# Performance work log

Hardware: AMD Instinct MI355X
Metric: run time of the kernel (lower is better)

Reference implementation:

```python
import jax, jax.numpy as jnp
import numpy as np

N = 50000
E = 800000
IN_C = 128
HID_C = 128
OUT_C = 128
N_CLS = 40


def setup_inputs() -> dict:
    key = jax.random.key(0)
    ks = jax.random.split(key, 12)
    x = jax.random.normal(ks[0], (N, IN_C), dtype=jnp.float32)
    edge_index = jax.random.randint(ks[1], (2, E), 0, N, dtype=jnp.int64)
    s = 1.0 / np.sqrt(IN_C)
    W_l1 = jax.random.uniform(ks[2], (IN_C, HID_C), jnp.float32, -s, s)
    W_r1 = jax.random.uniform(ks[3], (IN_C, HID_C), jnp.float32, -s, s)
    b1 = jax.random.uniform(ks[4], (HID_C,), jnp.float32, -s, s)
    s2 = 1.0 / np.sqrt(HID_C)
    W_l2 = jax.random.uniform(ks[5], (HID_C, OUT_C), jnp.float32, -s2, s2)
    W_r2 = jax.random.uniform(ks[6], (HID_C, OUT_C), jnp.float32, -s2, s2)
    b2 = jax.random.uniform(ks[7], (OUT_C,), jnp.float32, -s2, s2)
    s3 = 1.0 / np.sqrt(OUT_C)
    W_c = jax.random.uniform(ks[8], (OUT_C, N_CLS), jnp.float32, -s3, s3)
    b_c = jax.random.uniform(ks[9], (N_CLS,), jnp.float32, -s3, s3)
    return {"x": x, "edge_index": edge_index, "W_l1": W_l1, "W_r1": W_r1,
            "b1": b1, "W_l2": W_l2, "W_r2": W_r2, "b2": b2,
            "W_c": W_c, "b_c": b_c}


def _mean_aggregate(x, src, dst, deg_inv):
    # gather source node features over edges, scatter-mean to dst nodes
    msg = x[src]  # [E, C]
    agg = jax.ops.segment_sum(msg, dst, num_segments=N)  # [N, C]
    return agg * deg_inv[:, None]


def _sage_conv(x, src, dst, deg_inv, W_l, W_r, b):
    # PyG SAGEConv (mean aggr): out = agg @ W_l + x @ W_r + b
    agg = _mean_aggregate(x, src, dst, deg_inv)
    return agg @ W_l + x @ W_r + b


def reference(x, edge_index, W_l1, W_r1, b1, W_l2, W_r2, b2, W_c, b_c):
    src, dst = edge_index[0], edge_index[1]
    deg = jax.ops.segment_sum(jnp.ones((E,), jnp.float32), dst, num_segments=N)
    deg_inv = jnp.where(deg > 0, 1.0 / jnp.maximum(deg, 1.0), 0.0)
    h = jax.nn.relu(_sage_conv(x, src, dst, deg_inv, W_l1, W_r1, b1))
    h = jax.nn.relu(_sage_conv(h, src, dst, deg_inv, W_l2, W_r2, b2))
    return h @ W_c + b_c
```

## Files before the change

kernel.cpp:

```cpp
#include <hip/hip_runtime.h>

#define N_NODES 50000
#define N_EDGES 800000
#define C 128
#define NCLS 40
#define KB 98
#define BCAP 9216
#define WLD 264

typedef short bf16x8 __attribute__((ext_vector_type(8)));
typedef float f32x4 __attribute__((ext_vector_type(4)));
typedef unsigned short ushort_t;

__device__ __forceinline__ unsigned short f32_to_bf16(float f) {
    union { float f; unsigned u; } c; c.f = f;
    unsigned r = (c.u + 0x7FFFu + ((c.u >> 16) & 1u)) >> 16;
    return (unsigned short)r;
}
__device__ __forceinline__ float bf_lo(unsigned u) {
    union { unsigned u; float f; } c; c.u = u << 16; return c.f;
}
__device__ __forceinline__ float bf_hi(unsigned u) {
    union { unsigned u; float f; } c; c.u = u & 0xffff0000u; return c.f;
}
__device__ __forceinline__ unsigned pack_bf16(float lo, float hi) {
    return (unsigned)f32_to_bf16(lo) | ((unsigned)f32_to_bf16(hi) << 16);
}
__device__ __forceinline__ bf16x8 as_bf(uint4 u) {
    union { uint4 u; bf16x8 b; } c; c.u = u; return c.b;
}
__device__ __forceinline__ void acc8(float* a, uint4 v) {
    a[0] += bf_lo(v.x); a[1] += bf_hi(v.x); a[2] += bf_lo(v.y); a[3] += bf_hi(v.y);
    a[4] += bf_lo(v.z); a[5] += bf_hi(v.z); a[6] += bf_lo(v.w); a[7] += bf_hi(v.w);
}
__device__ __forceinline__ void acc8m(float* a, uint4 v, float mk) {
    a[0] += mk * bf_lo(v.x); a[1] += mk * bf_hi(v.x); a[2] += mk * bf_lo(v.y); a[3] += mk * bf_hi(v.y);
    a[4] += mk * bf_lo(v.z); a[5] += mk * bf_hi(v.z); a[6] += mk * bf_lo(v.w); a[7] += mk * bf_hi(v.w);
}

__global__ __launch_bounds__(256)
void convert_all(const float* __restrict__ Wl1, const float* __restrict__ Wr1,
                 const float* __restrict__ Wl2, const float* __restrict__ Wr2,
                 const float* __restrict__ Wc,  const float* __restrict__ x,
                 ushort_t* __restrict__ Wbf1, ushort_t* __restrict__ Wbf2,
                 ushort_t* __restrict__ Wcb,  ushort_t* __restrict__ xb) {
    int b = blockIdx.x;
    int tid = threadIdx.x;
    if (b < 256) {
        const float* Wl = (b < 128) ? Wl1 : Wl2;
        const float* Wr = (b < 128) ? Wr1 : Wr2;
        ushort_t* Bpre  = (b < 128) ? Wbf1 : Wbf2;
        int idx = (b & 127) * 256 + tid;
        int n = idx >> 8;
        int k = idx & 255;
        float v = (k < 128) ? Wl[k * 128 + n] : Wr[(k - 128) * 128 + n];
        Bpre[n * 256 + k] = f32_to_bf16(v);
    } else if (b < 280) {
        int idx = (b - 256) * 256 + tid;
        if (idx < 48 * 128) {
            int n = idx >> 7;
            int k = idx & 127;
            float v = (n < NCLS) ? Wc[k * NCLS + n] : 0.f;
            Wcb[idx] = f32_to_bf16(v);
        }
    } else {
        int idx = (b - 280) * 256 + tid;
        const float4 v0 = *(const float4*)&x[idx * 8];
        const float4 v1 = *(const float4*)&x[idx * 8 + 4];
        uint4 o;
        o.x = pack_bf16(v0.x, v0.y);
        o.y = pack_bf16(v0.z, v0.w);
        o.z = pack_bf16(v1.x, v1.y);
        o.w = pack_bf16(v1.z, v1.w);
        ((uint4*)xb)[idx] = o;
    }
}

__global__ __launch_bounds__(256)
void bin_kernel(const int* __restrict__ src, const int* __restrict__ dst,
                int* __restrict__ bucket_cnt, unsigned* __restrict__ bucket_data) {
    __shared__ int lh[KB];
    int tid = threadIdx.x;
    int e0 = blockIdx.x * 4096;
    if (tid < KB) lh[tid] = 0;
    __syncthreads();
#pragma unroll
    for (int j = 0; j < 16; ++j) {
        int e = e0 + j * 256 + tid;
        if (e < N_EDGES) atomicAdd(&lh[dst[e] >> 9], 1);
    }
    __syncthreads();
    if (tid < KB) lh[tid] = atomicAdd(&bucket_cnt[tid], lh[tid]);
    __syncthreads();
#pragma unroll
    for (int j = 0; j < 16; ++j) {
        int e = e0 + j * 256 + tid;
        if (e < N_EDGES) {
            int d = dst[e];
            int b = d >> 9;
            int pos = atomicAdd(&lh[b], 1);
            if (pos < BCAP)
                bucket_data[b * BCAP + pos] = (unsigned)src[e] | ((unsigned)(d & 511) << 16);
        }
    }
}

__global__ __launch_bounds__(256)
void build_kernel(const int* __restrict__ bucket_cnt, const unsigned* __restrict__ bucket_data,
                  int* __restrict__ row_ptr, ushort_t* __restrict__ csr16,
                  int* __restrict__ perm) {
    __shared__ int wt[4];
    __shared__ int wt2[4];
    __shared__ int sbases[128];
    __shared__ int hist[512];
    __shared__ int loff[512];
    __shared__ int dhist[64];
    __shared__ ushort_t lcsr[BCAP];
    int tid = threadIdx.x;
    int b = blockIdx.x;
    int n0 = b << 9;
    int nb = min(512, N_NODES - n0);

    int v = 0, x = 0;
    if (tid < 128) {
        v = (tid < KB) ? bucket_cnt[tid] : 0;
        x = v;
#pragma unroll
        for (int off = 1; off < 64; off <<= 1) {
            int t = __shfl_up(x, off, 64);
            if ((tid & 63) >= off) x += t;
        }
        if ((tid & 63) == 63) wt[tid >> 6] = x;
    }
    hist[tid] = 0; hist[tid + 256] = 0;
    __syncthreads();
    if (tid < 128) sbases[tid] = x - v + ((tid >= 64) ? wt[0] : 0);
    __syncthreads();
    int base = sbases[b];
    int ecnt = min(bucket_cnt[b], BCAP);

    for (int i = tid; i < ecnt; i += 256)
        atomicAdd(&hist[bucket_data[b * BCAP + i] >> 16], 1);
    __syncthreads();

    int h0 = hist[2 * tid], h1 = hist[2 * tid + 1];
    int s = h0 + h1;
    int y = s;
#pragma unroll
    for (int off = 1; off < 64; off <<= 1) {
        int t = __shfl_up(y, off, 64);
        if ((tid & 63) >= off) y += t;
    }
    if ((tid & 63) == 63) wt2[tid >> 6] = y;
    __syncthreads();
    int add = 0;
    for (int j = 0; j < (tid >> 6); ++j) add += wt2[j];
    int ex = y + add - s;
    loff[2 * tid] = ex;
    loff[2 * tid + 1] = ex + h0;
    __syncthreads();

    for (int n = tid; n < nb; n += 256) row_ptr[n0 + n] = base + loff[n];
    if (b == KB - 1 && tid == 0) row_ptr[N_NODES] = N_EDGES;
    __syncthreads();

    for (int i = tid; i < ecnt; i += 256) {
        unsigned e = bucket_data[b * BCAP + i];
        int pos = atomicAdd(&loff[e >> 16], 1);
        lcsr[pos] = (ushort_t)(e & 0xFFFFu);
    }
    __syncthreads();
    for (int i = tid; i < ecnt; i += 256) csr16[base + i] = lcsr[i];

    if (tid < 64) dhist[tid] = 0;
    for (int p = tid; p < 512; p += 256) perm[(b << 9) + p] = -1;
    __syncthreads();
    int na = 2 * tid, nbb = 2 * tid + 1;
    int c0 = min(h0, 63), c1 = min(h1, 63);
    if (na < nb)  atomicAdd(&dhist[c0], 1);
    if (nbb < nb) atomicAdd(&dhist[c1], 1);
    __syncthreads();
    if (tid < 64) {
        int v2 = dhist[tid];
        int xs = v2;
#pragma unroll
        for (int off = 1; off < 64; off <<= 1) {
            int t = __shfl_up(xs, off, 64);
            if (tid >= off) xs += t;
        }
        dhist[tid] = xs - v2;
    }
    __syncthreads();
    if (na < nb)  { int pos = atomicAdd(&dhist[c0], 1); perm[(b << 9) + pos] = n0 + na; }
    if (nbb < nb) { int pos = atomicAdd(&dhist[c1], 1); perm[(b << 9) + pos] = n0 + nbb; }
}

__global__ __launch_bounds__(256)
void gather_kernel(const ushort_t* __restrict__ feat,
                   const int* __restrict__ row_ptr,
                   const ushort_t* __restrict__ csr16,
                   const int* __restrict__ perm,
                   ushort_t* __restrict__ agg) {
    const int tid = threadIdx.x;
    const int q = tid & 15;
    const int g = tid >> 4;
    int slot = blockIdx.x * 16 + g;
    int node = perm[slot];
    if (node < 0) return;
    int beg = row_ptr[node], end = row_ptr[node + 1];
    int deg = end - beg;
    const uint4* fb = (const uint4*)feat;

    float a0[8], a1[8], a2[8], a3[8];
#pragma unroll
    for (int j = 0; j < 8; ++j) { a0[j] = 0.f; a1[j] = 0.f; a2[j] = 0.f; a3[j] = 0.f; }

    int n8 = deg >> 3;
    int s0 = 0, s1 = 0, s2 = 0, s3 = 0, s4 = 0, s5 = 0, s6 = 0, s7 = 0;
    if (n8 > 0) {
        s0 = csr16[beg];     s1 = csr16[beg + 1]; s2 = csr16[beg + 2]; s3 = csr16[beg + 3];
        s4 = csr16[beg + 4]; s5 = csr16[beg + 5]; s6 = csr16[beg + 6]; s7 = csr16[beg + 7];
    }
    for (int it = 0; it < n8; ++it) {
        uint4 v0 = fb[s0 * 16 + q];
        uint4 v1 = fb[s1 * 16 + q];
        uint4 v2 = fb[s2 * 16 + q];
        uint4 v3 = fb[s3 * 16 + q];
        uint4 v4 = fb[s4 * 16 + q];
        uint4 v5 = fb[s5 * 16 + q];
        uint4 v6 = fb[s6 * 16 + q];
        uint4 v7 = fb[s7 * 16 + q];
        if (it + 1 < n8) {
            int bs = beg + (it + 1) * 8;
            s0 = csr16[bs];     s1 = csr16[bs + 1]; s2 = csr16[bs + 2]; s3 = csr16[bs + 3];
            s4 = csr16[bs + 4]; s5 = csr16[bs + 5]; s6 = csr16[bs + 6]; s7 = csr16[bs + 7];
        }
        acc8(a0, v0); acc8(a1, v1); acc8(a2, v2); acc8(a3, v3);
        acc8(a0, v4); acc8(a1, v5); acc8(a2, v6); acc8(a3, v7);
    }
    int i = beg + n8 * 8;
    if (i + 4 <= end) {
        int t0 = csr16[i], t1 = csr16[i + 1], t2 = csr16[i + 2], t3 = csr16[i + 3];
        uint4 v0 = fb[t0 * 16 + q];
        uint4 v1 = fb[t1 * 16 + q];
        uint4 v2 = fb[t2 * 16 + q];
        uint4 v3 = fb[t3 * 16 + q];
        acc8(a0, v0); acc8(a1, v1); acc8(a2, v2); acc8(a3, v3);
        i += 4;
    }
    int rem = end - i;
    if (rem > 0) {
        int t0 = csr16[i];
        int t1 = csr16[i + (rem > 1 ? 1 : 0)];
        int t2 = csr16[i + (rem > 2 ? 2 : 0)];
        uint4 v0 = fb[t0 * 16 + q];
        uint4 v1 = fb[t1 * 16 + q];
        uint4 v2 = fb[t2 * 16 + q];
        acc8(a0, v0);
        acc8m(a1, v1, rem > 1 ? 1.f : 0.f);
        acc8m(a2, v2, rem > 2 ? 1.f : 0.f);
    }
    float di = deg > 0 ? 1.f / (float)deg : 0.f;
    float r[8];
#pragma unroll
    for (int j = 0; j < 8; ++j) r[j] = (a0[j] + a1[j] + a2[j] + a3[j]) * di;
    uint4 o;
    o.x = pack_bf16(r[0], r[1]);
    o.y = pack_bf16(r[2], r[3]);
    o.z = pack_bf16(r[4], r[5]);
    o.w = pack_bf16(r[6], r[7]);
    *(uint4*)&agg[node * C + q * 8] = o;
}

#define HLD 136
template<int CLS>
__global__ __launch_bounds__(256)
void gemm_layer(const ushort_t* __restrict__ agg,
                const ushort_t* __restrict__ feat,
                const ushort_t* __restrict__ Bpre,
                const float* __restrict__ bias,
                ushort_t* __restrict__ hout,
                const ushort_t* __restrict__ Wcb,
                const float* __restrict__ bc,
                float* __restrict__ out) {
    __shared__ ushort_t Wlds[128 * WLD];
    const int tid = threadIdx.x;
    const int r0 = blockIdx.x * 64;
    const int w = tid >> 6, lane = tid & 63, m = lane & 15, quad = lane >> 4;

#pragma unroll
    for (int i = 0; i < 16; ++i) {
        int idx = i * 256 + tid;
        int row = idx >> 5, c32 = idx & 31;
        *(uint4*)&Wlds[row * WLD + c32 * 8] = *(const uint4*)&Bpre[row * 256 + c32 * 8];
    }

    int rg = r0 + w * 16 + m; if (rg >= N_NODES) rg = N_NODES - 1;
    uint4 afa[4], aff[4];
#pragma unroll
    for (int kc = 0; kc < 4; ++kc) afa[kc] = *(const uint4*)&agg[rg * C + kc * 32 + quad * 8];
#pragma unroll
    for (int kc = 0; kc < 4; ++kc) aff[kc] = *(const uint4*)&feat[rg * C + kc * 32 + quad * 8];

    __syncthreads();

    f32x4 acc[8];
#pragma unroll
    for (int t = 0; t < 8; ++t) acc[t] = (f32x4){0.f, 0.f, 0.f, 0.f};

#pragma unroll
    for (int kc = 0; kc < 8; ++kc) {
        bf16x8 af = (kc < 4) ? as_bf(afa[kc]) : as_bf(aff[kc - 4]);
#pragma unroll
        for (int t = 0; t < 8; ++t) {
            bf16x8 bf = *(const bf16x8*)&Wlds[(t * 16 + m) * WLD + kc * 32 + quad * 8];
            acc[t] = __builtin_amdgcn_mfma_f32_16x16x32_bf16(af, bf, acc[t], 0, 0, 0);
        }
    }

    if (CLS == 0) {
#pragma unroll
        for (int t = 0; t < 8; ++t) {
            int colv = t * 16 + m;
            float bv = bias[colv];
#pragma unroll
            for (int reg = 0; reg < 4; ++reg) {
                int rs = r0 + w * 16 + quad * 4 + reg;
                if (rs < N_NODES) {
                    float vv = fmaxf(acc[t][reg] + bv, 0.f);
                    hout[rs * C + colv] = f32_to_bf16(vv);
                }
            }
        }
    } else {
        ushort_t* h2L = Wlds;
        ushort_t* WcL = Wlds + 64 * HLD;
        __syncthreads();
#pragma unroll
        for (int t = 0; t < 8; ++t) {
            int colv = t * 16 + m;
            float bv = bias[colv];
#pragma unroll
            for (int reg = 0; reg < 4; ++reg) {
                int rl = w * 16 + quad * 4 + reg;
                float vv = fmaxf(acc[t][reg] + bv, 0.f);
                h2L[rl * HLD + colv] = f32_to_bf16(vv);
            }
        }
#pragma unroll
        for (int i = 0; i < 3; ++i) {
            int slot = tid + i * 256;
            int n = slot >> 4, c16 = slot & 15;
            *(uint4*)&WcL[n * HLD + c16 * 8] = *(const uint4*)&Wcb[n * C + c16 * 8];
        }
        __syncthreads();
        f32x4 acc2[3];
#pragma unroll
        for (int t = 0; t < 3; ++t) acc2[t] = (f32x4){0.f, 0.f, 0.f, 0.f};
#pragma unroll
        for (int kc = 0; kc < 4; ++kc) {
            bf16x8 af = *(const bf16x8*)&h2L[(w * 16 + m) * HLD + kc * 32 + quad * 8];
#pragma unroll
            for (int t = 0; t < 3; ++t) {
                bf16x8 bf = *(const bf16x8*)&WcL[(t * 16 + m) * HLD + kc * 32 + quad * 8];
                acc2[t] = __builtin_amdgcn_mfma_f32_16x16x32_bf16(af, bf, acc2[t], 0, 0, 0);
            }
        }
#pragma unroll
        for (int t = 0; t < 3; ++t) {
            int col = t * 16 + m;
            if (col < NCLS) {
                float bvv = bc[col];
#pragma unroll
                for (int reg = 0; reg < 4; ++reg) {
                    int rs = r0 + w * 16 + quad * 4 + reg;
                    if (rs < N_NODES) out[rs * NCLS + col] = acc2[t][reg] + bvv;
                }
            }
        }
    }
}

extern "C" void kernel_launch(void* const* d_in, const int* in_sizes, int n_in,
                              void* d_out, int out_size, void* d_ws, size_t ws_size,
                              hipStream_t stream) {
    const float* x   = (const float*)d_in[0];
    const int*   ei  = (const int*)d_in[1];
    const float* Wl1 = (const float*)d_in[2];
    const float* Wr1 = (const float*)d_in[3];
    const float* b1  = (const float*)d_in[4];
    const float* Wl2 = (const float*)d_in[5];
    const float* Wr2 = (const float*)d_in[6];
    const float* b2  = (const float*)d_in[7];
    const float* Wc  = (const float*)d_in[8];
    const float* bc  = (const float*)d_in[9];
    const int* srcI = ei;
    const int* dstI = ei + N_EDGES;
    float* out = (float*)d_out;

    ushort_t* xb   = (ushort_t*)d_ws;
    ushort_t* h1b  = xb + (size_t)N_NODES * C;
    ushort_t* Wbf1 = h1b + (size_t)N_NODES * C;
    ushort_t* Wbf2 = Wbf1 + 32768;
    ushort_t* Wcb  = Wbf2 + 32768;
    ushort_t* csr16 = Wcb + 6144;
    int* bucket_cnt = (int*)(csr16 + N_EDGES);
    int* row_ptr    = bucket_cnt + 128;
    unsigned* bucket_data = (unsigned*)(row_ptr + N_NODES + 1);
    int* perm = (int*)(bucket_data + (size_t)KB * BCAP);
    ushort_t* aggb = (ushort_t*)(perm + KB * 512);

    convert_all<<<280 + (N_NODES * C / 8 + 255) / 256, 256, 0, stream>>>(
        Wl1, Wr1, Wl2, Wr2, Wc, x, Wbf1, Wbf2, Wcb, xb);

    hipMemsetAsync(bucket_cnt, 0, 128 * sizeof(int), stream);
    bin_kernel<<<(N_EDGES + 4095) / 4096, 256, 0, stream>>>(srcI, dstI, bucket_cnt, bucket_data);
    build_kernel<<<KB, 256, 0, stream>>>(bucket_cnt, bucket_data, row_ptr, csr16, perm);

    gather_kernel<<<KB * 512 / 16, 256, 0, stream>>>(xb, row_ptr, csr16, perm, aggb);
    gemm_layer<0><<<(N_NODES + 63) / 64, 256, 0, stream>>>(
        aggb, xb, Wbf1, b1, h1b, nullptr, nullptr, nullptr);

    gather_kernel<<<KB * 512 / 16, 256, 0, stream>>>(h1b, row_ptr, csr16, perm, aggb);
    gemm_layer<1><<<(N_NODES + 63) / 64, 256, 0, stream>>>(
        aggb, h1b, Wbf2, b2, nullptr, Wcb, bc, out);
}
```

Before: 222.1 us.

## Globally degree-sort nodes, source-sort CSR rows, and persist gather blocks over interleaved tiles

Node ordering for the gather now comes from a global degree histogram. A scan kernel and an atomic perm kernel replace the per-bucket degree sort, so nodes of similar degree are grouped across the whole graph. The build kernel also counting-sorts each bucket's edges by the high byte of the source id before placing them into CSR, so neighbor reads within a row touch nearby feature rows. The gather kernel now runs 784 blocks, each handling four 16-node groups taken from interleaved tiles, with launch bounds set for occupancy. This adds two small launches, a perm memset and extra shared memory in build in exchange for better load balance and locality.

```diff
diff --git a/kernel.cpp b/kernel.cpp
--- a/kernel.cpp
+++ b/kernel.cpp
@@ -7,6 +7,7 @@
 #define KB 98
 #define BCAP 9216
 #define WLD 264
+#define NPERM 50176
 
 typedef short bf16x8 __attribute__((ext_vector_type(8)));
 typedef float f32x4 __attribute__((ext_vector_type(4)));
@@ -108,13 +109,15 @@
 __global__ __launch_bounds__(256)
 void build_kernel(const int* __restrict__ bucket_cnt, const unsigned* __restrict__ bucket_data,
                   int* __restrict__ row_ptr, ushort_t* __restrict__ csr16,
-                  int* __restrict__ perm) {
+                  int* __restrict__ ghist) {
     __shared__ int wt[4];
     __shared__ int wt2[4];
     __shared__ int sbases[128];
     __shared__ int hist[512];
     __shared__ int loff[512];
-    __shared__ int dhist[64];
+    __shared__ int shist[256];
+    __shared__ int scur[256];
+    __shared__ unsigned sorted[BCAP];
     __shared__ ushort_t lcsr[BCAP];
     int tid = threadIdx.x;
     int b = blockIdx.x;
@@ -132,15 +135,41 @@
         }
         if ((tid & 63) == 63) wt[tid >> 6] = x;
     }
-    hist[tid] = 0; hist[tid + 256] = 0;
+    hist[tid] = 0; hist[tid + 256] = 0; shist[tid] = 0;
     __syncthreads();
     if (tid < 128) sbases[tid] = x - v + ((tid >= 64) ? wt[0] : 0);
     __syncthreads();
     int base = sbases[b];
     int ecnt = min(bucket_cnt[b], BCAP);
 
-    for (int i = tid; i < ecnt; i += 256)
-        atomicAdd(&hist[bucket_data[b * BCAP + i] >> 16], 1);
+    for (int i = tid; i < ecnt; i += 256) {
+        unsigned rec = bucket_data[b * BCAP + i];
+        atomicAdd(&shist[(rec & 0xFFFFu) >> 8], 1);
+        atomicAdd(&hist[rec >> 16], 1);
+    }
+    __syncthreads();
+
+    {
+        int v2 = shist[tid];
+        int y2 = v2;
+#pragma unroll
+        for (int off = 1; off < 64; off <<= 1) {
+            int t = __shfl_up(y2, off, 64);
+            if ((tid & 63) >= off) y2 += t;
+        }
+        if ((tid & 63) == 63) wt2[tid >> 6] = y2;
+        __syncthreads();
+        int add = 0;
+        for (int j = 0; j < (tid >> 6); ++j) add += wt2[j];
+        scur[tid] = y2 + add - v2;
+    }
+    __syncthreads();
+
+    for (int i = tid; i < ecnt; i += 256) {
+        unsigned rec = bucket_data[b * BCAP + i];
+        int pos = atomicAdd(&scur[(rec & 0xFFFFu) >> 8], 1);
+        sorted[pos] = rec;
+    }
     __syncthreads();
 
     int h0 = hist[2 * tid], h1 = hist[2 * tid + 1];
@@ -165,37 +194,41 @@
     __syncthreads();
 
     for (int i = tid; i < ecnt; i += 256) {
-        unsigned e = bucket_data[b * BCAP + i];
-        int pos = atomicAdd(&loff[e >> 16], 1);
-        lcsr[pos] = (ushort_t)(e & 0xFFFFu);
+        unsigned rec = sorted[i];
+        int pos = atomicAdd(&loff[rec >> 16], 1);
+        lcsr[pos] = (ushort_t)(rec & 0xFFFFu);
     }
     __syncthreads();
     for (int i = tid; i < ecnt; i += 256) csr16[base + i] = lcsr[i];
 
-    if (tid < 64) dhist[tid] = 0;
-    for (int p = tid; p < 512; p += 256) perm[(b << 9) + p] = -1;
-    __syncthreads();
-    int na = 2 * tid, nbb = 2 * tid + 1;
-    int c0 = min(h0, 63), c1 = min(h1, 63);
-    if (na < nb)  atomicAdd(&dhist[c0], 1);
-    if (nbb < nb) atomicAdd(&dhist[c1], 1);
-    __syncthreads();
-    if (tid < 64) {
-        int v2 = dhist[tid];
-        int xs = v2;
-#pragma unroll
-        for (int off = 1; off < 64; off <<= 1) {
-            int t = __shfl_up(xs, off, 64);
-            if (tid >= off) xs += t;
-        }
-        dhist[tid] = xs - v2;
-    }
-    __syncthreads();
-    if (na < nb)  { int pos = atomicAdd(&dhist[c0], 1); perm[(b << 9) + pos] = n0 + na; }
-    if (nbb < nb) { int pos = atomicAdd(&dhist[c1], 1); perm[(b << 9) + pos] = n0 + nbb; }
+    if (2 * tid < nb)     atomicAdd(&ghist[min(h0, 63)], 1);
+    if (2 * tid + 1 < nb) atomicAdd(&ghist[min(h1, 63)], 1);
+}
+
+__global__ void scan_kernel(const int* __restrict__ ghist, int* __restrict__ gcur) {
+    int t = threadIdx.x;
+    int v = ghist[t];
+    int x = v;
+#pragma unroll
+    for (int off = 1; off < 64; off <<= 1) {
+        int u = __shfl_up(x, off, 64);
+        if (t >= off) x += u;
+    }
+    gcur[t] = x - v;
 }
 
 __global__ __launch_bounds__(256)
+void perm_kernel(const int* __restrict__ row_ptr, int* __restrict__ gcur,
+                 int* __restrict__ perm) {
+    int n = blockIdx.x * 256 + threadIdx.x;
+    if (n < N_NODES) {
+        int deg = row_ptr[n + 1] - row_ptr[n];
+        int pos = atomicAdd(&gcur[min(deg, 63)], 1);
+        perm[pos] = n;
+    }
+}
+
+__global__ __launch_bounds__(256, 4)
 void gather_kernel(const ushort_t* __restrict__ feat,
                    const int* __restrict__ row_ptr,
                    const ushort_t* __restrict__ csr16,
@@ -204,72 +237,77 @@
     const int tid = threadIdx.x;
     const int q = tid & 15;
     const int g = tid >> 4;
-    int slot = blockIdx.x * 16 + g;
-    int node = perm[slot];
-    if (node < 0) return;
-    int beg = row_ptr[node], end = row_ptr[node + 1];
-    int deg = end - beg;
+    int bid = blockIdx.x;
+    int r0 = ((bid & 7) * 98 + (bid >> 3)) * 64;
     const uint4* fb = (const uint4*)feat;
 
-    float a0[8], a1[8], a2[8], a3[8];
-#pragma unroll
-    for (int j = 0; j < 8; ++j) { a0[j] = 0.f; a1[j] = 0.f; a2[j] = 0.f; a3[j] = 0.f; }
-
-    int n8 = deg >> 3;
-    int s0 = 0, s1 = 0, s2 = 0, s3 = 0, s4 = 0, s5 = 0, s6 = 0, s7 = 0;
-    if (n8 > 0) {
-        s0 = csr16[beg];     s1 = csr16[beg + 1]; s2 = csr16[beg + 2]; s3 = csr16[beg + 3];
-        s4 = csr16[beg + 4]; s5 = csr16[beg + 5]; s6 = csr16[beg + 6]; s7 = csr16[beg + 7];
-    }
-    for (int it = 0; it < n8; ++it) {
-        uint4 v0 = fb[s0 * 16 + q];
-        uint4 v1 = fb[s1 * 16 + q];
-        uint4 v2 = fb[s2 * 16 + q];
-        uint4 v3 = fb[s3 * 16 + q];
-        uint4 v4 = fb[s4 * 16 + q];
-        uint4 v5 = fb[s5 * 16 + q];
-        uint4 v6 = fb[s6 * 16 + q];
-        uint4 v7 = fb[s7 * 16 + q];
-        if (it + 1 < n8) {
-            int bs = beg + (it + 1) * 8;
-            s0 = csr16[bs];     s1 = csr16[bs + 1]; s2 = csr16[bs + 2]; s3 = csr16[bs + 3];
-            s4 = csr16[bs + 4]; s5 = csr16[bs + 5]; s6 = csr16[bs + 6]; s7 = csr16[bs + 7];
-        }
-        acc8(a0, v0); acc8(a1, v1); acc8(a2, v2); acc8(a3, v3);
-        acc8(a0, v4); acc8(a1, v5); acc8(a2, v6); acc8(a3, v7);
-    }
-    int i = beg + n8 * 8;
-    if (i + 4 <= end) {
-        int t0 = csr16[i], t1 = csr16[i + 1], t2 = csr16[i + 2], t3 = csr16[i + 3];
-        uint4 v0 = fb[t0 * 16 + q];
-        uint4 v1 = fb[t1 * 16 + q];
-        uint4 v2 = fb[t2 * 16 + q];
-        uint4 v3 = fb[t3 * 16 + q];
-        acc8(a0, v0); acc8(a1, v1); acc8(a2, v2); acc8(a3, v3);
-        i += 4;
-    }
-    int rem = end - i;
-    if (rem > 0) {
-        int t0 = csr16[i];
-        int t1 = csr16[i + (rem > 1 ? 1 : 0)];
-        int t2 = csr16[i + (rem > 2 ? 2 : 0)];
-        uint4 v0 = fb[t0 * 16 + q];
-        uint4 v1 = fb[t1 * 16 + q];
-        uint4 v2 = fb[t2 * 16 + q];
-        acc8(a0, v0);
-        acc8m(a1, v1, rem > 1 ? 1.f : 0.f);
-        acc8m(a2, v2, rem > 2 ? 1.f : 0.f);
-    }
-    float di = deg > 0 ? 1.f / (float)deg : 0.f;
-    float r[8];
-#pragma unroll
-    for (int j = 0; j < 8; ++j) r[j] = (a0[j] + a1[j] + a2[j] + a3[j]) * di;
-    uint4 o;
-    o.x = pack_bf16(r[0], r[1]);
-    o.y = pack_bf16(r[2], r[3]);
-    o.z = pack_bf16(r[4], r[5]);
-    o.w = pack_bf16(r[6], r[7]);
-    *(uint4*)&agg[node * C + q * 8] = o;
+    for (int p = 0; p < 4; ++p) {
+        int node = perm[r0 + p * 16 + g];
+        if (node >= 0) {
+            int beg = row_ptr[node], end = row_ptr[node + 1];
+            int deg = end - beg;
+
+            float a0[8], a1[8], a2[8], a3[8];
+#pragma unroll
+            for (int j = 0; j < 8; ++j) { a0[j] = 0.f; a1[j] = 0.f; a2[j] = 0.f; a3[j] = 0.f; }
+
+            int n8 = deg >> 3;
+            int s0 = 0, s1 = 0, s2 = 0, s3 = 0, s4 = 0, s5 = 0, s6 = 0, s7 = 0;
+            if (n8 > 0) {
+                s0 = csr16[beg];     s1 = csr16[beg + 1]; s2 = csr16[beg + 2]; s3 = csr16[beg + 3];
+                s4 = csr16[beg + 4]; s5 = csr16[beg + 5]; s6 = csr16[beg + 6]; s7 = csr16[beg + 7];
+            }
+            for (int it = 0; it < n8; ++it) {
+                uint4 v0 = fb[s0 * 16 + q];
+                uint4 v1 = fb[s1 * 16 + q];
+                uint4 v2 = fb[s2 * 16 + q];
+                uint4 v3 = fb[s3 * 16 + q];
+                uint4 v4 = fb[s4 * 16 + q];
+                uint4 v5 = fb[s5 * 16 + q];
+                uint4 v6 = fb[s6 * 16 + q];
+                uint4 v7 = fb[s7 * 16 + q];
+                if (it + 1 < n8) {
+                    int bs = beg + (it + 1) * 8;
+                    s0 = csr16[bs];     s1 = csr16[bs + 1]; s2 = csr16[bs + 2]; s3 = csr16[bs + 3];
+                    s4 = csr16[bs + 4]; s5 = csr16[bs + 5]; s6 = csr16[bs + 6]; s7 = csr16[bs + 7];
+                }
+                acc8(a0, v0); acc8(a1, v1); acc8(a2, v2); acc8(a3, v3);
+                acc8(a0, v4); acc8(a1, v5); acc8(a2, v6); acc8(a3, v7);
+            }
+            int i = beg + n8 * 8;
+            if (i + 4 <= end) {
+                int t0 = csr16[i], t1 = csr16[i + 1], t2 = csr16[i + 2], t3 = csr16[i + 3];
+                uint4 v0 = fb[t0 * 16 + q];
+                uint4 v1 = fb[t1 * 16 + q];
+                uint4 v2 = fb[t2 * 16 + q];
+                uint4 v3 = fb[t3 * 16 + q];
+                acc8(a0, v0); acc8(a1, v1); acc8(a2, v2); acc8(a3, v3);
+                i += 4;
+            }
+            int rem = end - i;
+            if (rem > 0) {
+                int t0 = csr16[i];
+                int t1 = csr16[i + (rem > 1 ? 1 : 0)];
+                int t2 = csr16[i + (rem > 2 ? 2 : 0)];
+                uint4 v0 = fb[t0 * 16 + q];
+                uint4 v1 = fb[t1 * 16 + q];
+                uint4 v2 = fb[t2 * 16 + q];
+                acc8(a0, v0);
+                acc8m(a1, v1, rem > 1 ? 1.f : 0.f);
+                acc8m(a2, v2, rem > 2 ? 1.f : 0.f);
+            }
+            float di = deg > 0 ? 1.f / (float)deg : 0.f;
+            float r[8];
+#pragma unroll
+            for (int j = 0; j < 8; ++j) r[j] = (a0[j] + a1[j] + a2[j] + a3[j]) * di;
+            uint4 o;
+            o.x = pack_bf16(r[0], r[1]);
+            o.y = pack_bf16(r[2], r[3]);
+            o.z = pack_bf16(r[4], r[5]);
+            o.w = pack_bf16(r[6], r[7]);
+            *(uint4*)&agg[node * C + q * 8] = o;
+        }
+    }
 }
 
 #define HLD 136
@@ -405,23 +443,28 @@
     ushort_t* Wcb  = Wbf2 + 32768;
     ushort_t* csr16 = Wcb + 6144;
     int* bucket_cnt = (int*)(csr16 + N_EDGES);
-    int* row_ptr    = bucket_cnt + 128;
+    int* ghist      = bucket_cnt + 128;
+    int* gcur       = ghist + 64;
+    int* row_ptr    = gcur + 64;
     unsigned* bucket_data = (unsigned*)(row_ptr + N_NODES + 1);
     int* perm = (int*)(bucket_data + (size_t)KB * BCAP);
-    ushort_t* aggb = (ushort_t*)(perm + KB * 512);
+    ushort_t* aggb = (ushort_t*)(perm + NPERM);
 
     convert_all<<<280 + (N_NODES * C / 8 + 255) / 256, 256, 0, stream>>>(
         Wl1, Wr1, Wl2, Wr2, Wc, x, Wbf1, Wbf2, Wcb, xb);
 
-    hipMemsetAsync(bucket_cnt, 0, 128 * sizeof(int), stream);
+    hipMemsetAsync(bucket_cnt, 0, 256 * sizeof(int), stream);
+    hipMemsetAsync(perm, 0xFF, NPERM * sizeof(int), stream);
     bin_kernel<<<(N_EDGES + 4095) / 4096, 256, 0, stream>>>(srcI, dstI, bucket_cnt, bucket_data);
-    build_kernel<<<KB, 256, 0, stream>>>(bucket_cnt, bucket_data, row_ptr, csr16, perm);
-
-    gather_kernel<<<KB * 512 / 16, 256, 0, stream>>>(xb, row_ptr, csr16, perm, aggb);
+    build_kernel<<<KB, 256, 0, stream>>>(bucket_cnt, bucket_data, row_ptr, csr16, ghist);
+    scan_kernel<<<1, 64, 0, stream>>>(ghist, gcur);
+    perm_kernel<<<(N_NODES + 255) / 256, 256, 0, stream>>>(row_ptr, gcur, perm);
+
+    gather_kernel<<<784, 256, 0, stream>>>(xb, row_ptr, csr16, perm, aggb);
     gemm_layer<0><<<(N_NODES + 63) / 64, 256, 0, stream>>>(
         aggb, xb, Wbf1, b1, h1b, nullptr, nullptr, nullptr);
 
-    gather_kernel<<<KB * 512 / 16, 256, 0, stream>>>(h1b, row_ptr, csr16, perm, aggb);
+    gather_kernel<<<784, 256, 0, stream>>>(h1b, row_ptr, csr16, perm, aggb);
     gemm_layer<1><<<(N_NODES + 63) / 64, 256, 0, stream>>>(
         aggb, h1b, Wbf2, b2, nullptr, Wcb, bc, out);
 }
```

Result: slower. 502.1 us (+126.0%).

## Fuse neighbor gather-mean with SAGE GEMM per 64-node tile via shared memory

Applied to the files above, without the earlier changes.

Merges the gather kernel and the GEMM kernel into one 512-thread kernel per layer. The kernel aggregates 64 permuted nodes into LDS and then runs the bf16 MFMA GEMM on them, streaming the weight K-slices through LDS. This removes the global round trip of the aggregate buffer and two launches. In exchange it adds a __syncthreads per K-chunk, gathers root features by scattered perm index, writes outputs by permuted row, and may lose occupancy. The classifier head is also redistributed across 8 waves.

```diff
diff --git a/kernel.cpp b/kernel.cpp
--- a/kernel.cpp
+++ b/kernel.cpp
@@ -6,7 +6,6 @@
 #define NCLS 40
 #define KB 98
 #define BCAP 9216
-#define WLD 264
 
 typedef short bf16x8 __attribute__((ext_vector_type(8)));
 typedef float f32x4 __attribute__((ext_vector_type(4)));
@@ -25,9 +24,6 @@
 }
 __device__ __forceinline__ unsigned pack_bf16(float lo, float hi) {
     return (unsigned)f32_to_bf16(lo) | ((unsigned)f32_to_bf16(hi) << 16);
-}
-__device__ __forceinline__ bf16x8 as_bf(uint4 u) {
-    union { uint4 u; bf16x8 b; } c; c.u = u; return c.b;
 }
 __device__ __forceinline__ void acc8(float* a, uint4 v) {
     a[0] += bf_lo(v.x); a[1] += bf_hi(v.x); a[2] += bf_lo(v.y); a[3] += bf_hi(v.y);
@@ -195,186 +191,198 @@
     if (nbb < nb) { int pos = atomicAdd(&dhist[c1], 1); perm[(b << 9) + pos] = n0 + nbb; }
 }
 
-__global__ __launch_bounds__(256)
-void gather_kernel(const ushort_t* __restrict__ feat,
-                   const int* __restrict__ row_ptr,
-                   const ushort_t* __restrict__ csr16,
-                   const int* __restrict__ perm,
-                   ushort_t* __restrict__ agg) {
-    const int tid = threadIdx.x;
-    const int q = tid & 15;
-    const int g = tid >> 4;
-    int slot = blockIdx.x * 16 + g;
-    int node = perm[slot];
-    if (node < 0) return;
-    int beg = row_ptr[node], end = row_ptr[node + 1];
-    int deg = end - beg;
-    const uint4* fb = (const uint4*)feat;
-
-    float a0[8], a1[8], a2[8], a3[8];
-#pragma unroll
-    for (int j = 0; j < 8; ++j) { a0[j] = 0.f; a1[j] = 0.f; a2[j] = 0.f; a3[j] = 0.f; }
-
-    int n8 = deg >> 3;
-    int s0 = 0, s1 = 0, s2 = 0, s3 = 0, s4 = 0, s5 = 0, s6 = 0, s7 = 0;
-    if (n8 > 0) {
-        s0 = csr16[beg];     s1 = csr16[beg + 1]; s2 = csr16[beg + 2]; s3 = csr16[beg + 3];
-        s4 = csr16[beg + 4]; s5 = csr16[beg + 5]; s6 = csr16[beg + 6]; s7 = csr16[beg + 7];
-    }
-    for (int it = 0; it < n8; ++it) {
-        uint4 v0 = fb[s0 * 16 + q];
-        uint4 v1 = fb[s1 * 16 + q];
-        uint4 v2 = fb[s2 * 16 + q];
-        uint4 v3 = fb[s3 * 16 + q];
-        uint4 v4 = fb[s4 * 16 + q];
-        uint4 v5 = fb[s5 * 16 + q];
-        uint4 v6 = fb[s6 * 16 + q];
-        uint4 v7 = fb[s7 * 16 + q];
-        if (it + 1 < n8) {
-            int bs = beg + (it + 1) * 8;
-            s0 = csr16[bs];     s1 = csr16[bs + 1]; s2 = csr16[bs + 2]; s3 = csr16[bs + 3];
-            s4 = csr16[bs + 4]; s5 = csr16[bs + 5]; s6 = csr16[bs + 6]; s7 = csr16[bs + 7];
-        }
-        acc8(a0, v0); acc8(a1, v1); acc8(a2, v2); acc8(a3, v3);
-        acc8(a0, v4); acc8(a1, v5); acc8(a2, v6); acc8(a3, v7);
-    }
-    int i = beg + n8 * 8;
-    if (i + 4 <= end) {
-        int t0 = csr16[i], t1 = csr16[i + 1], t2 = csr16[i + 2], t3 = csr16[i + 3];
-        uint4 v0 = fb[t0 * 16 + q];
-        uint4 v1 = fb[t1 * 16 + q];
-        uint4 v2 = fb[t2 * 16 + q];
-        uint4 v3 = fb[t3 * 16 + q];
-        acc8(a0, v0); acc8(a1, v1); acc8(a2, v2); acc8(a3, v3);
-        i += 4;
-    }
-    int rem = end - i;
-    if (rem > 0) {
-        int t0 = csr16[i];
-        int t1 = csr16[i + (rem > 1 ? 1 : 0)];
-        int t2 = csr16[i + (rem > 2 ? 2 : 0)];
-        uint4 v0 = fb[t0 * 16 + q];
-        uint4 v1 = fb[t1 * 16 + q];
-        uint4 v2 = fb[t2 * 16 + q];
-        acc8(a0, v0);
-        acc8m(a1, v1, rem > 1 ? 1.f : 0.f);
-        acc8m(a2, v2, rem > 2 ? 1.f : 0.f);
-    }
-    float di = deg > 0 ? 1.f / (float)deg : 0.f;
-    float r[8];
-#pragma unroll
-    for (int j = 0; j < 8; ++j) r[j] = (a0[j] + a1[j] + a2[j] + a3[j]) * di;
-    uint4 o;
-    o.x = pack_bf16(r[0], r[1]);
-    o.y = pack_bf16(r[2], r[3]);
-    o.z = pack_bf16(r[4], r[5]);
-    o.w = pack_bf16(r[6], r[7]);
-    *(uint4*)&agg[node * C + q * 8] = o;
-}
-
-#define HLD 136
+#define ALD 136
 template<int CLS>
-__global__ __launch_bounds__(256)
-void gemm_layer(const ushort_t* __restrict__ agg,
-                const ushort_t* __restrict__ feat,
-                const ushort_t* __restrict__ Bpre,
-                const float* __restrict__ bias,
-                ushort_t* __restrict__ hout,
-                const ushort_t* __restrict__ Wcb,
-                const float* __restrict__ bc,
-                float* __restrict__ out) {
-    __shared__ ushort_t Wlds[128 * WLD];
+__global__ __launch_bounds__(512)
+void fused_layer(const ushort_t* __restrict__ feat,
+                 const int* __restrict__ row_ptr,
+                 const ushort_t* __restrict__ csr16,
+                 const int* __restrict__ perm,
+                 const ushort_t* __restrict__ Bpre,
+                 const float* __restrict__ bias,
+                 ushort_t* __restrict__ hout,
+                 const ushort_t* __restrict__ Wcb,
+                 const float* __restrict__ bc,
+                 float* __restrict__ out) {
+    __shared__ ushort_t aggL[64 * ALD];
+    __shared__ ushort_t stg[64 * 40 + 128 * 40];
+    __shared__ int tperm[64];
+    ushort_t* AsX = stg;
+    ushort_t* BsP = stg + 64 * 40;
     const int tid = threadIdx.x;
     const int r0 = blockIdx.x * 64;
     const int w = tid >> 6, lane = tid & 63, m = lane & 15, quad = lane >> 4;
-
-#pragma unroll
-    for (int i = 0; i < 16; ++i) {
-        int idx = i * 256 + tid;
-        int row = idx >> 5, c32 = idx & 31;
-        *(uint4*)&Wlds[row * WLD + c32 * 8] = *(const uint4*)&Bpre[row * 256 + c32 * 8];
-    }
-
-    int rg = r0 + w * 16 + m; if (rg >= N_NODES) rg = N_NODES - 1;
-    uint4 afa[4], aff[4];
-#pragma unroll
-    for (int kc = 0; kc < 4; ++kc) afa[kc] = *(const uint4*)&agg[rg * C + kc * 32 + quad * 8];
-#pragma unroll
-    for (int kc = 0; kc < 4; ++kc) aff[kc] = *(const uint4*)&feat[rg * C + kc * 32 + quad * 8];
-
-    __syncthreads();
-
-    f32x4 acc[8];
-#pragma unroll
-    for (int t = 0; t < 8; ++t) acc[t] = (f32x4){0.f, 0.f, 0.f, 0.f};
-
-#pragma unroll
+    const int q = tid & 15;
+    const int g = tid >> 4;
+
+    if (tid < 64) tperm[tid] = perm[r0 + tid];
+    __syncthreads();
+
+    const uint4* fb = (const uint4*)feat;
+    for (int p = 0; p < 2; ++p) {
+        int nl = p * 32 + g;
+        int node = tperm[nl];
+        if (node >= 0) {
+            int beg = row_ptr[node], end = row_ptr[node + 1];
+            int deg = end - beg;
+            float a0[8], a1[8], a2[8], a3[8];
+#pragma unroll
+            for (int j = 0; j < 8; ++j) { a0[j] = 0.f; a1[j] = 0.f; a2[j] = 0.f; a3[j] = 0.f; }
+
+            int n8 = deg >> 3;
+            int s0 = 0, s1 = 0, s2 = 0, s3 = 0, s4 = 0, s5 = 0, s6 = 0, s7 = 0;
+            if (n8 > 0) {
+                s0 = csr16[beg];     s1 = csr16[beg + 1]; s2 = csr16[beg + 2]; s3 = csr16[beg + 3];
+                s4 = csr16[beg + 4]; s5 = csr16[beg + 5]; s6 = csr16[beg + 6]; s7 = csr16[beg + 7];
+            }
+            for (int it = 0; it < n8; ++it) {
+                uint4 v0 = fb[s0 * 16 + q];
+                uint4 v1 = fb[s1 * 16 + q];
+                uint4 v2 = fb[s2 * 16 + q];
+                uint4 v3 = fb[s3 * 16 + q];
+                uint4 v4 = fb[s4 * 16 + q];
+                uint4 v5 = fb[s5 * 16 + q];
+                uint4 v6 = fb[s6 * 16 + q];
+                uint4 v7 = fb[s7 * 16 + q];
+                if (it + 1 < n8) {
+                    int bs = beg + (it + 1) * 8;
+                    s0 = csr16[bs];     s1 = csr16[bs + 1]; s2 = csr16[bs + 2]; s3 = csr16[bs + 3];
+                    s4 = csr16[bs + 4]; s5 = csr16[bs + 5]; s6 = csr16[bs + 6]; s7 = csr16[bs + 7];
+                }
+                acc8(a0, v0); acc8(a1, v1); acc8(a2, v2); acc8(a3, v3);
+                acc8(a0, v4); acc8(a1, v5); acc8(a2, v6); acc8(a3, v7);
+            }
+            int i = beg + n8 * 8;
+            if (i + 4 <= end) {
+                int t0 = csr16[i], t1 = csr16[i + 1], t2 = csr16[i + 2], t3 = csr16[i + 3];
+                uint4 v0 = fb[t0 * 16 + q];
+                uint4 v1 = fb[t1 * 16 + q];
+                uint4 v2 = fb[t2 * 16 + q];
+                uint4 v3 = fb[t3 * 16 + q];
+                acc8(a0, v0); acc8(a1, v1); acc8(a2, v2); acc8(a3, v3);
+                i += 4;
+            }
+            int rem = end - i;
+            if (rem > 0) {
+                int t0 = csr16[i];
+                int t1 = csr16[i + (rem > 1 ? 1 : 0)];
+                int t2 = csr16[i + (rem > 2 ? 2 : 0)];
+                uint4 v0 = fb[t0 * 16 + q];
+                uint4 v1 = fb[t1 * 16 + q];
+                uint4 v2 = fb[t2 * 16 + q];
+                acc8(a0, v0);
+                acc8m(a1, v1, rem > 1 ? 1.f : 0.f);
+                acc8m(a2, v2, rem > 2 ? 1.f : 0.f);
+            }
+            float di = deg > 0 ? 1.f / (float)deg : 0.f;
+            float r[8];
+#pragma unroll
+            for (int j = 0; j < 8; ++j) r[j] = (a0[j] + a1[j] + a2[j] + a3[j]) * di;
+            uint4 o;
+            o.x = pack_bf16(r[0], r[1]);
+            o.y = pack_bf16(r[2], r[3]);
+            o.z = pack_bf16(r[4], r[5]);
+            o.w = pack_bf16(r[6], r[7]);
+            *(uint4*)&aggL[nl * ALD + q * 8] = o;
+        }
+    }
+    __syncthreads();
+
+    f32x4 acc[4];
+#pragma unroll
+    for (int t = 0; t < 4; ++t) acc[t] = (f32x4){0.f, 0.f, 0.f, 0.f};
+
     for (int kc = 0; kc < 8; ++kc) {
-        bf16x8 af = (kc < 4) ? as_bf(afa[kc]) : as_bf(aff[kc - 4]);
-#pragma unroll
-        for (int t = 0; t < 8; ++t) {
-            bf16x8 bf = *(const bf16x8*)&Wlds[(t * 16 + m) * WLD + kc * 32 + quad * 8];
-            acc[t] = __builtin_amdgcn_mfma_f32_16x16x32_bf16(af, bf, acc[t], 0, 0, 0);
+        if (kc) __syncthreads();
+        if (kc >= 4 && tid < 256) {
+            int row = tid >> 2;
+            int kq = tid & 3;
+            int nd = tperm[row]; if (nd < 0) nd = 0;
+            uint4 vv = *(const uint4*)&feat[nd * C + (kc & 3) * 32 + kq * 8];
+            *(uint4*)&AsX[row * 40 + kq * 8] = vv;
+        }
+        {
+            int n = tid >> 2;
+            int qq = tid & 3;
+            *(uint4*)&BsP[n * 40 + qq * 8] = *(const uint4*)&Bpre[n * 256 + kc * 32 + qq * 8];
+        }
+        __syncthreads();
+        bf16x8 bfr = *(const bf16x8*)&BsP[(w * 16 + m) * 40 + quad * 8];
+#pragma unroll
+        for (int rt = 0; rt < 4; ++rt) {
+            bf16x8 af = (kc < 4)
+                ? *(const bf16x8*)&aggL[(rt * 16 + m) * ALD + kc * 32 + quad * 8]
+                : *(const bf16x8*)&AsX[(rt * 16 + m) * 40 + quad * 8];
+            acc[rt] = __builtin_amdgcn_mfma_f32_16x16x32_bf16(af, bfr, acc[rt], 0, 0, 0);
         }
     }
 
     if (CLS == 0) {
-#pragma unroll
-        for (int t = 0; t < 8; ++t) {
-            int colv = t * 16 + m;
-            float bv = bias[colv];
+        int colv = w * 16 + m;
+        float bv = bias[colv];
+#pragma unroll
+        for (int rt = 0; rt < 4; ++rt) {
 #pragma unroll
             for (int reg = 0; reg < 4; ++reg) {
-                int rs = r0 + w * 16 + quad * 4 + reg;
-                if (rs < N_NODES) {
-                    float vv = fmaxf(acc[t][reg] + bv, 0.f);
-                    hout[rs * C + colv] = f32_to_bf16(vv);
+                int rg = tperm[rt * 16 + quad * 4 + reg];
+                if (rg >= 0) {
+                    float vv = fmaxf(acc[rt][reg] + bv, 0.f);
+                    hout[rg * C + colv] = f32_to_bf16(vv);
                 }
             }
         }
     } else {
-        ushort_t* h2L = Wlds;
-        ushort_t* WcL = Wlds + 64 * HLD;
         __syncthreads();
-#pragma unroll
-        for (int t = 0; t < 8; ++t) {
-            int colv = t * 16 + m;
-            float bv = bias[colv];
+        int colv = w * 16 + m;
+        float bv = bias[colv];
+#pragma unroll
+        for (int rt = 0; rt < 4; ++rt) {
 #pragma unroll
             for (int reg = 0; reg < 4; ++reg) {
-                int rl = w * 16 + quad * 4 + reg;
-                float vv = fmaxf(acc[t][reg] + bv, 0.f);
-                h2L[rl * HLD + colv] = f32_to_bf16(vv);
-            }
-        }
-#pragma unroll
-        for (int i = 0; i < 3; ++i) {
-            int slot = tid + i * 256;
-            int n = slot >> 4, c16 = slot & 15;
-            *(uint4*)&WcL[n * HLD + c16 * 8] = *(const uint4*)&Wcb[n * C + c16 * 8];
+                int rl = rt * 16 + quad * 4 + reg;
+                float vv = fmaxf(acc[rt][reg] + bv, 0.f);
+                aggL[rl * ALD + colv] = f32_to_bf16(vv);
+            }
+        }
+#pragma unroll
+        for (int i = 0; i < 2; ++i) {
+            int slot = tid + i * 512;
+            if (slot < 768) {
+                int n = slot >> 4, kq = slot & 15;
+                uint4 vv = *(const uint4*)&Wcb[n * C + kq * 8];
+                *(uint4*)&stg[(kq >> 2) * (48 * 40) + n * 40 + (kq & 3) * 8] = vv;
+            }
         }
         __syncthreads();
-        f32x4 acc2[3];
-#pragma unroll
-        for (int t = 0; t < 3; ++t) acc2[t] = (f32x4){0.f, 0.f, 0.f, 0.f};
+        int rtA = w & 3;
+        int ctA = (w < 4) ? 0 : 1;
+        f32x4 acc2a = (f32x4){0.f, 0.f, 0.f, 0.f};
+        f32x4 acc2b = (f32x4){0.f, 0.f, 0.f, 0.f};
 #pragma unroll
         for (int kc = 0; kc < 4; ++kc) {
-            bf16x8 af = *(const bf16x8*)&h2L[(w * 16 + m) * HLD + kc * 32 + quad * 8];
-#pragma unroll
-            for (int t = 0; t < 3; ++t) {
-                bf16x8 bf = *(const bf16x8*)&WcL[(t * 16 + m) * HLD + kc * 32 + quad * 8];
-                acc2[t] = __builtin_amdgcn_mfma_f32_16x16x32_bf16(af, bf, acc2[t], 0, 0, 0);
-            }
-        }
-#pragma unroll
-        for (int t = 0; t < 3; ++t) {
-            int col = t * 16 + m;
-            if (col < NCLS) {
-                float bvv = bc[col];
+            bf16x8 af = *(const bf16x8*)&aggL[(rtA * 16 + m) * ALD + kc * 32 + quad * 8];
+            bf16x8 bfA = *(const bf16x8*)&stg[kc * (48 * 40) + (ctA * 16 + m) * 40 + quad * 8];
+            acc2a = __builtin_amdgcn_mfma_f32_16x16x32_bf16(af, bfA, acc2a, 0, 0, 0);
+            if (w < 4) {
+                bf16x8 bfB = *(const bf16x8*)&stg[kc * (48 * 40) + (32 + m) * 40 + quad * 8];
+                acc2b = __builtin_amdgcn_mfma_f32_16x16x32_bf16(af, bfB, acc2b, 0, 0, 0);
+            }
+        }
+        int colA = ctA * 16 + m;
+        float bA = bc[colA];
+#pragma unroll
+        for (int reg = 0; reg < 4; ++reg) {
+            int rg = tperm[rtA * 16 + quad * 4 + reg];
+            if (rg >= 0) out[rg * NCLS + colA] = acc2a[reg] + bA;
+        }
+        if (w < 4) {
+            int colB = 32 + m;
+            if (colB < NCLS) {
+                float bB = bc[colB];
 #pragma unroll
                 for (int reg = 0; reg < 4; ++reg) {
-                    int rs = r0 + w * 16 + quad * 4 + reg;
-                    if (rs < N_NODES) out[rs * NCLS + col] = acc2[t][reg] + bvv;
+                    int rg = tperm[rtA * 16 + quad * 4 + reg];
+                    if (rg >= 0) out[rg * NCLS + colB] = acc2b[reg] + bB;
                 }
             }
         }
@@ -408,7 +416,6 @@
     int* row_ptr    = bucket_cnt + 128;
     unsigned* bucket_data = (unsigned*)(row_ptr + N_NODES + 1);
     int* perm = (int*)(bucket_data + (size_t)KB * BCAP);
-    ushort_t* aggb = (ushort_t*)(perm + KB * 512);
 
     convert_all<<<280 + (N_NODES * C / 8 + 255) / 256, 256, 0, stream>>>(
         Wl1, Wr1, Wl2, Wr2, Wc, x, Wbf1, Wbf2, Wcb, xb);
@@ -417,11 +424,9 @@
     bin_kernel<<<(N_EDGES + 4095) / 4096, 256, 0, stream>>>(srcI, dstI, bucket_cnt, bucket_data);
     build_kernel<<<KB, 256, 0, stream>>>(bucket_cnt, bucket_data, row_ptr, csr16, perm);
 
-    gather_kernel<<<KB * 512 / 16, 256, 0, stream>>>(xb, row_ptr, csr16, perm, aggb);
-    gemm_layer<0><<<(N_NODES + 63) / 64, 256, 0, stream>>>(
-        aggb, xb, Wbf1, b1, h1b, nullptr, nullptr, nullptr);
-
-    gather_kernel<<<KB * 512 / 16, 256, 0, stream>>>(h1b, row_ptr, csr16, perm, aggb);
-    gemm_layer<1><<<(N_NODES + 63) / 64, 256, 0, stream>>>(
-        aggb, h1b, Wbf2, b2, nullptr, Wcb, bc, out);
-}
+    fused_layer<0><<<KB * 8, 512, 0, stream>>>(
+        xb, row_ptr, csr16, perm, Wbf1, b1, h1b, nullptr, nullptr, nullptr);
+
+    fused_layer<1><<<KB * 8, 512, 0, stream>>>(
+        h1b, row_ptr, csr16, perm, Wbf2, b2, nullptr, Wcb, bc, out);
+}
```

New measurement: 223.4 us. Within noise of the previous version (+0.6%).
